# Performance work log

Hardware: AMD Instinct MI355X
Metric: run time of the kernel (lower is better)

The kernel has to match this reference:

```python
import jax, jax.numpy as jnp
import numpy as np

B = 16          # number of point clouds in the batch
N_COARSE = 1024 # coarse points per cloud
N_FINE = 4096   # fine (skip) points per cloud
C_IN = 256
C_SKIP = 128
K = 3
EPS = 1e-16


def setup_inputs() -> dict:
    key = jax.random.key(0)
    ks = jax.random.split(key, 8)
    x = jax.random.normal(ks[0], (B * N_COARSE, C_IN), dtype=jnp.float32)
    pos = jax.random.uniform(ks[1], (B * N_COARSE, 3), dtype=jnp.float32)
    x_skip = jax.random.normal(ks[2], (B * N_FINE, C_SKIP), dtype=jnp.float32)
    pos_skip = jax.random.uniform(ks[3], (B * N_FINE, 3), dtype=jnp.float32)
    batch = jnp.repeat(jnp.arange(B, dtype=jnp.int64), N_COARSE)
    batch_skip = jnp.repeat(jnp.arange(B, dtype=jnp.int64), N_FINE)
    W1 = jax.random.normal(ks[4], (C_IN + C_SKIP, 256), dtype=jnp.float32) * (1.0 / np.sqrt(C_IN + C_SKIP))
    b1 = jnp.zeros((256,), dtype=jnp.float32)
    W2 = jax.random.normal(ks[5], (256, 256), dtype=jnp.float32) * (1.0 / np.sqrt(256))
    b2 = jnp.zeros((256,), dtype=jnp.float32)
    return {"x": x, "pos": pos, "batch": batch, "x_skip": x_skip,
            "pos_skip": pos_skip, "batch_skip": batch_skip,
            "W1": W1, "b1": b1, "W2": W2, "b2": b2}


def _knn_interpolate(x, pos, pos_skip):
    # Equal-sized clouds: reshape to [B, N, *] and do batched kNN.
    xc = x.reshape(B, N_COARSE, C_IN)
    pc = pos.reshape(B, N_COARSE, 3)
    pf = pos_skip.reshape(B, N_FINE, 3)
    # squared pairwise distances [B, M, N]
    d2 = (jnp.sum(pf * pf, -1)[:, :, None]
          + jnp.sum(pc * pc, -1)[:, None, :]
          - 2.0 * jnp.einsum('bmd,bnd->bmn', pf, pc))
    d2 = jnp.maximum(d2, 0.0)
    neg_d2k, idx = jax.lax.top_k(-d2, K)          # k smallest distances
    w = 1.0 / jnp.maximum(-neg_d2k, EPS)          # [B, M, K] inverse-sq-dist weights
    gathered = jax.vmap(lambda f, i: f[i])(xc, idx)  # [B, M, K, C]
    y = jnp.sum(w[..., None] * gathered, axis=2) / jnp.sum(w, axis=2, keepdims=True)
    return y.reshape(B * N_FINE, C_IN)


def reference(x, pos, batch, x_skip, pos_skip, batch_skip, W1, b1, W2, b2):
    x_interp = _knn_interpolate(x, pos, pos_skip)          # [B*M, C_IN]
    h = jnp.concatenate([x_interp, x_skip], axis=1)        # [B*M, C_IN + C_SKIP]
    h = jax.nn.relu(h @ W1 + b1)
    out = jax.nn.relu(h @ W2 + b2)
    return out
```

## Files before the change

kernel.cpp:

```cpp
#include <hip/hip_runtime.h>

typedef float  f32x4  __attribute__((ext_vector_type(4)));
typedef short  short8 __attribute__((ext_vector_type(8)));
typedef unsigned short ushort_t;
typedef ushort_t us4   __attribute__((ext_vector_type(4)));

#define NCOARSE 1024
#define NFINE   4096

#define GLL16(g, l)                                                   \
  __builtin_amdgcn_global_load_lds(                                   \
      (__attribute__((address_space(1))) void*)(g),                   \
      (__attribute__((address_space(3))) void*)(l), 16, 0, 0)

__device__ __forceinline__ ushort_t f2bf(float f){
  union { float f; unsigned u; } a; a.f = f;
  unsigned u = a.u;
  return (ushort_t)((u + 0x7fffu + ((u >> 16) & 1u)) >> 16);
}

__device__ __forceinline__ f32x4 splat4(float v){ f32x4 t = {v, v, v, v}; return t; }

__global__ void prep_w2(const float* __restrict__ W1, const float* __restrict__ W2,
                        ushort_t* __restrict__ W1p, ushort_t* __restrict__ W2p){
  int e = blockIdx.x * 256 + threadIdx.x;
  const float* W; ushort_t* Wp; int idx;
  if (e < 98304){ W = W1; Wp = W1p; idx = e; }
  else          { W = W2; Wp = W2p; idx = e - 98304; }
  int j    = idx & 7;
  int lane = (idx >> 3) & 63;
  int g    = idx >> 9;
  int nb   = g & 15;
  int kc   = g >> 4;
  int k = kc * 32 + (lane >> 4) * 8 + j;
  int n = nb * 16 + (lane & 15);
  Wp[idx] = f2bf(W[k * 256 + n]);
}

__global__ __launch_bounds__(256) void knn_kernel(const float* __restrict__ pos,
                           const float* __restrict__ pos_skip,
                           int* __restrict__ knn_i, float* __restrict__ knn_w){
  __shared__ f32x4 cand[8][129];
  const int tid = threadIdx.x;
  const int b   = blockIdx.x >> 7;
  const int m   = blockIdx.x * 32 + (tid >> 3);
  const int chunk = tid & 7;

  const float* p = pos + (size_t)b * NCOARSE * 3;
  for (int c = tid; c < NCOARSE; c += 256){
    float x = p[3*c], y = p[3*c+1], z = p[3*c+2];
    float sc = __fadd_rn(__fadd_rn(__fmul_rn(x,x), __fmul_rn(y,y)), __fmul_rn(z,z));
    f32x4 v = { x, y, z, sc };
    cand[c >> 7][c & 127] = v;
  }
  __syncthreads();

  const float* q = pos_skip + (size_t)m * 3;
  float qx = q[0], qy = q[1], qz = q[2];
  float sf = __fadd_rn(__fadd_rn(__fmul_rn(qx,qx), __fmul_rn(qy,qy)), __fmul_rn(qz,qz));

  float d0 = 1e30f, d1 = 1e30f, d2 = 1e30f;
  int   i0 = 0,     i1 = 0,     i2 = 0;
  const int gbase = chunk * 128;
  #pragma unroll 4
  for (int i = 0; i < 128; ++i){
    f32x4 v = cand[chunk][i];
    float dot = __fadd_rn(__fadd_rn(__fmul_rn(qx, v.x), __fmul_rn(qy, v.y)),
                          __fmul_rn(qz, v.z));
    float d = __fsub_rn(__fadd_rn(sf, v.w), __fmul_rn(2.0f, dot));
    d = fmaxf(d, 0.0f);
    if (d < d2){
      int gi = gbase + i;
      if (d < d1){
        d2 = d1; i2 = i1;
        if (d < d0){ d1 = d0; i1 = i0; d0 = d; i0 = gi; }
        else       { d1 = d;  i1 = gi; }
      } else { d2 = d; i2 = gi; }
    }
  }

  #pragma unroll
  for (int mlev = 1; mlev <= 4; mlev <<= 1){
    float e0 = __shfl_xor(d0, mlev), e1 = __shfl_xor(d1, mlev), e2 = __shfl_xor(d2, mlev);
    int   j0 = __shfl_xor(i0, mlev), j1 = __shfl_xor(i1, mlev), j2 = __shfl_xor(i2, mlev);
    #pragma unroll
    for (int s = 0; s < 3; ++s){
      float e = (s == 0) ? e0 : (s == 1) ? e1 : e2;
      int   j = (s == 0) ? j0 : (s == 1) ? j1 : j2;
      bool l2 = (e < d2) || (e == d2 && j < i2);
      if (l2){
        bool l1 = (e < d1) || (e == d1 && j < i1);
        if (l1){
          d2 = d1; i2 = i1;
          bool l0 = (e < d0) || (e == d0 && j < i0);
          if (l0){ d1 = d0; i1 = i0; d0 = e; i0 = j; }
          else   { d1 = e;  i1 = j; }
        } else { d2 = e; i2 = j; }
      }
    }
  }

  if (chunk == 0){
    float w0 = 1.0f / fmaxf(d0, 1e-16f);
    float w1 = 1.0f / fmaxf(d1, 1e-16f);
    float w2 = 1.0f / fmaxf(d2, 1e-16f);
    float ws = __fadd_rn(__fadd_rn(w0, w1), w2);
    knn_i[3*m]   = b * NCOARSE + i0;
    knn_i[3*m+1] = b * NCOARSE + i1;
    knn_i[3*m+2] = b * NCOARSE + i2;
    knn_w[3*m]   = w0 / ws;
    knn_w[3*m+1] = w1 / ws;
    knn_w[3*m+2] = w2 / ws;
  }
}

__global__ __launch_bounds__(256, 2)
void fused_fp(const float* __restrict__ x, const float* __restrict__ x_skip,
              const int* __restrict__ knn_i, const float* __restrict__ knn_w,
              const ushort_t* __restrict__ W1p, const float* __restrict__ b1,
              const ushort_t* __restrict__ W2p, const float* __restrict__ b2,
              float* __restrict__ out){
  __shared__ __align__(16) ushort_t hbuf[32 * 384];
  __shared__ __align__(16) ushort_t wbuf[3][8192];
  char* h1b = (char*)hbuf;
  char* h2b = (char*)hbuf;
  const int tid  = threadIdx.x;
  const int lb   = ((blockIdx.x & 7) << 8) + (blockIdx.x >> 3);
  const int row0 = lb * 32;
  const int wp   = tid >> 6;
  const int lane = tid & 63;
  const int lhi  = lane >> 4;
  const int llo  = lane & 15;

  auto stageW = [&](int s){
    const ushort_t* Wsel = (s < 12) ? W1p : W2p;
    int fbase = ((s < 12) ? s : (s - 12)) * 16 + wp * 4;
    #pragma unroll
    for (int i = 0; i < 4; ++i){
      const ushort_t* g = Wsel + (size_t)(fbase + i) * 512 + lane * 8;
      ushort_t* l = &wbuf[s % 3][(wp * 4 + i) * 512];
      GLL16(g, l);
    }
  };

  stageW(0);
  stageW(1);

  {
    const int r   = tid >> 3;
    const int sub = tid & 7;
    const int m   = row0 + r;
    const f32x4* xsr = (const f32x4*)(x_skip + (size_t)m * 128);
    f32x4 xs[4];
    #pragma unroll
    for (int it = 0; it < 4; ++it) xs[it] = xsr[it * 8 + sub];
    int i0 = knn_i[3*m], i1 = knn_i[3*m+1], i2 = knn_i[3*m+2];
    float w0 = knn_w[3*m], w1 = knn_w[3*m+1], w2 = knn_w[3*m+2];
    const f32x4* x0 = (const f32x4*)(x + (size_t)i0 * 256);
    const f32x4* x1 = (const f32x4*)(x + (size_t)i1 * 256);
    const f32x4* x2 = (const f32x4*)(x + (size_t)i2 * 256);
    #pragma unroll
    for (int it = 0; it < 8; ++it){
      int c4 = it * 8 + sub;
      f32x4 v = x0[c4] * w0 + x1[c4] * w1 + x2[c4] * w2;
      int byte = (r * 768 + c4 * 8) ^ ((r & 7) << 4);
      us4 pk = { f2bf(v.x), f2bf(v.y), f2bf(v.z), f2bf(v.w) };
      *(us4*)(h1b + byte) = pk;
    }
    #pragma unroll
    for (int it = 0; it < 4; ++it){
      int c4 = it * 8 + sub;
      f32x4 v = xs[it];
      int byte = (r * 768 + 512 + c4 * 8) ^ ((r & 7) << 4);
      us4 pk = { f2bf(v.x), f2bf(v.y), f2bf(v.z), f2bf(v.w) };
      *(us4*)(h1b + byte) = pk;
    }
  }
  __syncthreads();

  f32x4 acc[2][4];
  #pragma unroll
  for (int nbp = 0; nbp < 4; ++nbp){
    float bb = b1[wp * 64 + nbp * 16 + llo];
    #pragma unroll
    for (int mb = 0; mb < 2; ++mb) acc[mb][nbp] = splat4(bb);
  }
  #pragma unroll
  for (int kk = 0; kk < 12; ++kk){
    asm volatile("s_waitcnt vmcnt(4)" ::: "memory");
    __builtin_amdgcn_s_barrier();
    asm volatile("" ::: "memory");
    stageW(kk + 2);
    short8 af[2];
    #pragma unroll
    for (int mb = 0; mb < 2; ++mb){
      int rr = mb * 16 + llo;
      int byte = (rr * 768 + kk * 64 + lhi * 16) ^ ((rr & 7) << 4);
      af[mb] = *(const short8*)(h1b + byte);
    }
    short8 wf[4];
    #pragma unroll
    for (int nbp = 0; nbp < 4; ++nbp)
      wf[nbp] = *(const short8*)&wbuf[kk % 3][(wp * 4 + nbp) * 512 + lane * 8];
    #pragma unroll
    for (int mb = 0; mb < 2; ++mb)
      #pragma unroll
      for (int nbp = 0; nbp < 4; ++nbp)
        acc[mb][nbp] = __builtin_amdgcn_mfma_f32_16x16x32_bf16(
            af[mb], wf[nbp], acc[mb][nbp], 0, 0, 0);
  }
  __syncthreads();

  #pragma unroll
  for (int mb = 0; mb < 2; ++mb)
    #pragma unroll
    for (int nbp = 0; nbp < 4; ++nbp)
      #pragma unroll
      for (int rg = 0; rg < 4; ++rg){
        int rr  = mb * 16 + lhi * 4 + rg;
        int col = wp * 64 + nbp * 16 + llo;
        int byte = (rr * 512 + col * 2) ^ ((rr & 7) << 4);
        *(ushort_t*)(h2b + byte) = f2bf(fmaxf(acc[mb][nbp][rg], 0.0f));
      }
  __syncthreads();

  f32x4 acc2[2][4];
  #pragma unroll
  for (int nbp = 0; nbp < 4; ++nbp){
    float bb = b2[wp * 64 + nbp * 16 + llo];
    #pragma unroll
    for (int mb = 0; mb < 2; ++mb) acc2[mb][nbp] = splat4(bb);
  }
  #pragma unroll
  for (int t = 0; t < 8; ++t){
    const int s = 12 + t;
    if (t < 7) { asm volatile("s_waitcnt vmcnt(4)" ::: "memory"); }
    else       { asm volatile("s_waitcnt vmcnt(0)" ::: "memory"); }
    __builtin_amdgcn_s_barrier();
    asm volatile("" ::: "memory");
    if (t < 6) stageW(s + 2);
    short8 af[2];
    #pragma unroll
    for (int mb = 0; mb < 2; ++mb){
      int rr = mb * 16 + llo;
      int byte = (rr * 512 + t * 64 + lhi * 16) ^ ((rr & 7) << 4);
      af[mb] = *(const short8*)(h2b + byte);
    }
    short8 wf[4];
    #pragma unroll
    for (int nbp = 0; nbp < 4; ++nbp)
      wf[nbp] = *(const short8*)&wbuf[s % 3][(wp * 4 + nbp) * 512 + lane * 8];
    #pragma unroll
    for (int mb = 0; mb < 2; ++mb)
      #pragma unroll
      for (int nbp = 0; nbp < 4; ++nbp)
        acc2[mb][nbp] = __builtin_amdgcn_mfma_f32_16x16x32_bf16(
            af[mb], wf[nbp], acc2[mb][nbp], 0, 0, 0);
  }

  #pragma unroll
  for (int mb = 0; mb < 2; ++mb)
    #pragma unroll
    for (int nbp = 0; nbp < 4; ++nbp)
      #pragma unroll
      for (int rg = 0; rg < 4; ++rg){
        int row = row0 + mb * 16 + lhi * 4 + rg;
        int col = wp * 64 + nbp * 16 + llo;
        out[(size_t)row * 256 + col] = fmaxf(acc2[mb][nbp][rg], 0.0f);
      }
}

extern "C" void kernel_launch(void* const* d_in, const int* in_sizes, int n_in,
                              void* d_out, int out_size, void* d_ws, size_t ws_size,
                              hipStream_t stream){
  (void)in_sizes; (void)n_in; (void)out_size; (void)ws_size;
  const float* x        = (const float*)d_in[0];
  const float* pos      = (const float*)d_in[1];
  const float* x_skip   = (const float*)d_in[3];
  const float* pos_skip = (const float*)d_in[4];
  const float* W1 = (const float*)d_in[6];
  const float* b1 = (const float*)d_in[7];
  const float* W2 = (const float*)d_in[8];
  const float* b2 = (const float*)d_in[9];
  float* out = (float*)d_out;
  char* ws = (char*)d_ws;
  ushort_t* W1p = (ushort_t*)(ws);
  ushort_t* W2p = (ushort_t*)(ws + 196608);
  int*      ki  = (int*)(ws + 327680);
  float*    kw  = (float*)(ws + 1114112);

  hipLaunchKernelGGL(prep_w2, dim3(640), dim3(256), 0, stream, W1, W2, W1p, W2p);
  hipLaunchKernelGGL(knn_kernel, dim3(2048), dim3(256), 0, stream, pos, pos_skip, ki, kw);
  hipLaunchKernelGGL(fused_fp, dim3(2048), dim3(256), 0, stream,
                     x, x_skip, ki, kw, W1p, b1, W2p, b2, out);
}
```

Before: 96.09 us.

## Fuse kNN search into MLP kernel and load weights directly to registers

Merges the kNN kernel into the fused MLP kernel. Each block now computes its own 32 rows' three nearest neighbours in shared memory, then reuses the same buffer for the activations, so the neighbour index and weight arrays no longer round-trip through global memory and one launch goes away. Weight fragments are also loaded straight from global memory into a three-deep register ring instead of being staged through LDS with barriers, and occupancy is raised to three blocks per CU. The risks are more register pressure and each block repeating the candidate-table load for its cloud.

```diff
diff --git a/kernel.cpp b/kernel.cpp
--- a/kernel.cpp
+++ b/kernel.cpp
@@ -7,11 +7,6 @@
 
 #define NCOARSE 1024
 #define NFINE   4096
-
-#define GLL16(g, l)                                                   \
-  __builtin_amdgcn_global_load_lds(                                   \
-      (__attribute__((address_space(1))) void*)(g),                   \
-      (__attribute__((address_space(3))) void*)(l), 16, 0, 0)
 
 __device__ __forceinline__ ushort_t f2bf(float f){
   union { float f; unsigned u; } a; a.f = f;
@@ -37,132 +32,115 @@
   Wp[idx] = f2bf(W[k * 256 + n]);
 }
 
-__global__ __launch_bounds__(256) void knn_kernel(const float* __restrict__ pos,
-                           const float* __restrict__ pos_skip,
-                           int* __restrict__ knn_i, float* __restrict__ knn_w){
-  __shared__ f32x4 cand[8][129];
-  const int tid = threadIdx.x;
-  const int b   = blockIdx.x >> 7;
-  const int m   = blockIdx.x * 32 + (tid >> 3);
-  const int chunk = tid & 7;
-
-  const float* p = pos + (size_t)b * NCOARSE * 3;
-  for (int c = tid; c < NCOARSE; c += 256){
-    float x = p[3*c], y = p[3*c+1], z = p[3*c+2];
-    float sc = __fadd_rn(__fadd_rn(__fmul_rn(x,x), __fmul_rn(y,y)), __fmul_rn(z,z));
-    f32x4 v = { x, y, z, sc };
-    cand[c >> 7][c & 127] = v;
-  }
-  __syncthreads();
-
-  const float* q = pos_skip + (size_t)m * 3;
-  float qx = q[0], qy = q[1], qz = q[2];
-  float sf = __fadd_rn(__fadd_rn(__fmul_rn(qx,qx), __fmul_rn(qy,qy)), __fmul_rn(qz,qz));
-
-  float d0 = 1e30f, d1 = 1e30f, d2 = 1e30f;
-  int   i0 = 0,     i1 = 0,     i2 = 0;
-  const int gbase = chunk * 128;
-  #pragma unroll 4
-  for (int i = 0; i < 128; ++i){
-    f32x4 v = cand[chunk][i];
-    float dot = __fadd_rn(__fadd_rn(__fmul_rn(qx, v.x), __fmul_rn(qy, v.y)),
-                          __fmul_rn(qz, v.z));
-    float d = __fsub_rn(__fadd_rn(sf, v.w), __fmul_rn(2.0f, dot));
-    d = fmaxf(d, 0.0f);
-    if (d < d2){
-      int gi = gbase + i;
-      if (d < d1){
-        d2 = d1; i2 = i1;
-        if (d < d0){ d1 = d0; i1 = i0; d0 = d; i0 = gi; }
-        else       { d1 = d;  i1 = gi; }
-      } else { d2 = d; i2 = gi; }
-    }
-  }
-
-  #pragma unroll
-  for (int mlev = 1; mlev <= 4; mlev <<= 1){
-    float e0 = __shfl_xor(d0, mlev), e1 = __shfl_xor(d1, mlev), e2 = __shfl_xor(d2, mlev);
-    int   j0 = __shfl_xor(i0, mlev), j1 = __shfl_xor(i1, mlev), j2 = __shfl_xor(i2, mlev);
-    #pragma unroll
-    for (int s = 0; s < 3; ++s){
-      float e = (s == 0) ? e0 : (s == 1) ? e1 : e2;
-      int   j = (s == 0) ? j0 : (s == 1) ? j1 : j2;
-      bool l2 = (e < d2) || (e == d2 && j < i2);
-      if (l2){
-        bool l1 = (e < d1) || (e == d1 && j < i1);
-        if (l1){
+#define LDW4(DST, WP, STEP)                                                   \
+  { _Pragma("unroll")                                                         \
+    for (int n_ = 0; n_ < 4; ++n_)                                            \
+      DST[n_] = *(const short8*)((WP) +                                       \
+          ((size_t)(((STEP) * 16 + wp * 4 + n_) * 64 + lane)) * 8); }
+
+__global__ __launch_bounds__(256, 3)
+void fp_fused(const float* __restrict__ pos, const float* __restrict__ pos_skip,
+              const float* __restrict__ x, const float* __restrict__ x_skip,
+              const ushort_t* __restrict__ W1p, const float* __restrict__ b1,
+              const ushort_t* __restrict__ W2p, const float* __restrict__ b2,
+              float* __restrict__ out){
+  __shared__ __align__(16) ushort_t hbuf[32 * 384];
+  char* h1b = (char*)hbuf;
+  char* h2b = (char*)hbuf;
+  f32x4* candp = (f32x4*)hbuf;
+  const int tid  = threadIdx.x;
+  const int lb   = ((blockIdx.x & 7) << 8) + (blockIdx.x >> 3);
+  const int row0 = lb * 32;
+  const int b    = lb >> 7;
+  const int wp   = tid >> 6;
+  const int lane = tid & 63;
+  const int lhi  = lane >> 4;
+  const int llo  = lane & 15;
+  const int r    = tid >> 3;
+  const int sub  = tid & 7;
+
+  {
+    const float* p = pos + (size_t)b * NCOARSE * 3;
+    for (int c = tid; c < NCOARSE; c += 256){
+      float xx = p[3*c], yy = p[3*c+1], zz = p[3*c+2];
+      float sc = __fadd_rn(__fadd_rn(__fmul_rn(xx,xx), __fmul_rn(yy,yy)), __fmul_rn(zz,zz));
+      f32x4 v = { xx, yy, zz, sc };
+      candp[(c >> 7) * 129 + (c & 127)] = v;
+    }
+  }
+  __syncthreads();
+
+  float wn0, wn1, wn2;
+  int   ig0, ig1, ig2;
+  {
+    const int m = row0 + r;
+    const float* q = pos_skip + (size_t)m * 3;
+    float qx = q[0], qy = q[1], qz = q[2];
+    float sf = __fadd_rn(__fadd_rn(__fmul_rn(qx,qx), __fmul_rn(qy,qy)), __fmul_rn(qz,qz));
+
+    float d0 = 1e30f, d1 = 1e30f, d2 = 1e30f;
+    int   i0 = 0,     i1 = 0,     i2 = 0;
+    const int gbase = sub * 128;
+    #pragma unroll 4
+    for (int i = 0; i < 128; ++i){
+      f32x4 v = candp[sub * 129 + i];
+      float dot = __fadd_rn(__fadd_rn(__fmul_rn(qx, v.x), __fmul_rn(qy, v.y)),
+                            __fmul_rn(qz, v.z));
+      float d = __fsub_rn(__fadd_rn(sf, v.w), __fmul_rn(2.0f, dot));
+      d = fmaxf(d, 0.0f);
+      if (d < d2){
+        int gi = gbase + i;
+        if (d < d1){
           d2 = d1; i2 = i1;
-          bool l0 = (e < d0) || (e == d0 && j < i0);
-          if (l0){ d1 = d0; i1 = i0; d0 = e; i0 = j; }
-          else   { d1 = e;  i1 = j; }
-        } else { d2 = e; i2 = j; }
-      }
-    }
-  }
-
-  if (chunk == 0){
+          if (d < d0){ d1 = d0; i1 = i0; d0 = d; i0 = gi; }
+          else       { d1 = d;  i1 = gi; }
+        } else { d2 = d; i2 = gi; }
+      }
+    }
+
+    #pragma unroll
+    for (int mlev = 1; mlev <= 4; mlev <<= 1){
+      float e0 = __shfl_xor(d0, mlev), e1 = __shfl_xor(d1, mlev), e2 = __shfl_xor(d2, mlev);
+      int   j0 = __shfl_xor(i0, mlev), j1 = __shfl_xor(i1, mlev), j2 = __shfl_xor(i2, mlev);
+      #pragma unroll
+      for (int s = 0; s < 3; ++s){
+        float e = (s == 0) ? e0 : (s == 1) ? e1 : e2;
+        int   j = (s == 0) ? j0 : (s == 1) ? j1 : j2;
+        bool l2 = (e < d2) || (e == d2 && j < i2);
+        if (l2){
+          bool l1 = (e < d1) || (e == d1 && j < i1);
+          if (l1){
+            d2 = d1; i2 = i1;
+            bool l0 = (e < d0) || (e == d0 && j < i0);
+            if (l0){ d1 = d0; i1 = i0; d0 = e; i0 = j; }
+            else   { d1 = e;  i1 = j; }
+          } else { d2 = e; i2 = j; }
+        }
+      }
+    }
+
     float w0 = 1.0f / fmaxf(d0, 1e-16f);
     float w1 = 1.0f / fmaxf(d1, 1e-16f);
     float w2 = 1.0f / fmaxf(d2, 1e-16f);
     float ws = __fadd_rn(__fadd_rn(w0, w1), w2);
-    knn_i[3*m]   = b * NCOARSE + i0;
-    knn_i[3*m+1] = b * NCOARSE + i1;
-    knn_i[3*m+2] = b * NCOARSE + i2;
-    knn_w[3*m]   = w0 / ws;
-    knn_w[3*m+1] = w1 / ws;
-    knn_w[3*m+2] = w2 / ws;
-  }
-}
-
-__global__ __launch_bounds__(256, 2)
-void fused_fp(const float* __restrict__ x, const float* __restrict__ x_skip,
-              const int* __restrict__ knn_i, const float* __restrict__ knn_w,
-              const ushort_t* __restrict__ W1p, const float* __restrict__ b1,
-              const ushort_t* __restrict__ W2p, const float* __restrict__ b2,
-              float* __restrict__ out){
-  __shared__ __align__(16) ushort_t hbuf[32 * 384];
-  __shared__ __align__(16) ushort_t wbuf[3][8192];
-  char* h1b = (char*)hbuf;
-  char* h2b = (char*)hbuf;
-  const int tid  = threadIdx.x;
-  const int lb   = ((blockIdx.x & 7) << 8) + (blockIdx.x >> 3);
-  const int row0 = lb * 32;
-  const int wp   = tid >> 6;
-  const int lane = tid & 63;
-  const int lhi  = lane >> 4;
-  const int llo  = lane & 15;
-
-  auto stageW = [&](int s){
-    const ushort_t* Wsel = (s < 12) ? W1p : W2p;
-    int fbase = ((s < 12) ? s : (s - 12)) * 16 + wp * 4;
-    #pragma unroll
-    for (int i = 0; i < 4; ++i){
-      const ushort_t* g = Wsel + (size_t)(fbase + i) * 512 + lane * 8;
-      ushort_t* l = &wbuf[s % 3][(wp * 4 + i) * 512];
-      GLL16(g, l);
-    }
-  };
-
-  stageW(0);
-  stageW(1);
-
-  {
-    const int r   = tid >> 3;
-    const int sub = tid & 7;
-    const int m   = row0 + r;
+    wn0 = w0 / ws; wn1 = w1 / ws; wn2 = w2 / ws;
+    ig0 = b * NCOARSE + i0; ig1 = b * NCOARSE + i1; ig2 = b * NCOARSE + i2;
+  }
+  __syncthreads();
+
+  {
+    const int m = row0 + r;
     const f32x4* xsr = (const f32x4*)(x_skip + (size_t)m * 128);
     f32x4 xs[4];
     #pragma unroll
     for (int it = 0; it < 4; ++it) xs[it] = xsr[it * 8 + sub];
-    int i0 = knn_i[3*m], i1 = knn_i[3*m+1], i2 = knn_i[3*m+2];
-    float w0 = knn_w[3*m], w1 = knn_w[3*m+1], w2 = knn_w[3*m+2];
-    const f32x4* x0 = (const f32x4*)(x + (size_t)i0 * 256);
-    const f32x4* x1 = (const f32x4*)(x + (size_t)i1 * 256);
-    const f32x4* x2 = (const f32x4*)(x + (size_t)i2 * 256);
+    const f32x4* x0 = (const f32x4*)(x + (size_t)ig0 * 256);
+    const f32x4* x1 = (const f32x4*)(x + (size_t)ig1 * 256);
+    const f32x4* x2 = (const f32x4*)(x + (size_t)ig2 * 256);
     #pragma unroll
     for (int it = 0; it < 8; ++it){
       int c4 = it * 8 + sub;
-      f32x4 v = x0[c4] * w0 + x1[c4] * w1 + x2[c4] * w2;
+      f32x4 v = x0[c4] * wn0 + x1[c4] * wn1 + x2[c4] * wn2;
       int byte = (r * 768 + c4 * 8) ^ ((r & 7) << 4);
       us4 pk = { f2bf(v.x), f2bf(v.y), f2bf(v.z), f2bf(v.w) };
       *(us4*)(h1b + byte) = pk;
@@ -185,29 +163,28 @@
     #pragma unroll
     for (int mb = 0; mb < 2; ++mb) acc[mb][nbp] = splat4(bb);
   }
-  #pragma unroll
-  for (int kk = 0; kk < 12; ++kk){
-    asm volatile("s_waitcnt vmcnt(4)" ::: "memory");
-    __builtin_amdgcn_s_barrier();
-    asm volatile("" ::: "memory");
-    stageW(kk + 2);
-    short8 af[2];
-    #pragma unroll
-    for (int mb = 0; mb < 2; ++mb){
-      int rr = mb * 16 + llo;
-      int byte = (rr * 768 + kk * 64 + lhi * 16) ^ ((rr & 7) << 4);
-      af[mb] = *(const short8*)(h1b + byte);
-    }
-    short8 wf[4];
-    #pragma unroll
-    for (int nbp = 0; nbp < 4; ++nbp)
-      wf[nbp] = *(const short8*)&wbuf[kk % 3][(wp * 4 + nbp) * 512 + lane * 8];
-    #pragma unroll
-    for (int mb = 0; mb < 2; ++mb)
-      #pragma unroll
-      for (int nbp = 0; nbp < 4; ++nbp)
-        acc[mb][nbp] = __builtin_amdgcn_mfma_f32_16x16x32_bf16(
-            af[mb], wf[nbp], acc[mb][nbp], 0, 0, 0);
+  {
+    short8 wr[3][4];
+    LDW4(wr[0], W1p, 0);
+    LDW4(wr[1], W1p, 1);
+    LDW4(wr[2], W1p, 2);
+    #pragma unroll
+    for (int kk = 0; kk < 12; ++kk){
+      short8 af[2];
+      #pragma unroll
+      for (int mb = 0; mb < 2; ++mb){
+        int rr = mb * 16 + llo;
+        int byte = (rr * 768 + kk * 64 + lhi * 16) ^ ((rr & 7) << 4);
+        af[mb] = *(const short8*)(h1b + byte);
+      }
+      #pragma unroll
+      for (int mb = 0; mb < 2; ++mb)
+        #pragma unroll
+        for (int nbp = 0; nbp < 4; ++nbp)
+          acc[mb][nbp] = __builtin_amdgcn_mfma_f32_16x16x32_bf16(
+              af[mb], wr[kk % 3][nbp], acc[mb][nbp], 0, 0, 0);
+      if (kk + 3 < 12) { LDW4(wr[kk % 3], W1p, kk + 3); }
+    }
   }
   __syncthreads();
 
@@ -231,31 +208,28 @@
     #pragma unroll
     for (int mb = 0; mb < 2; ++mb) acc2[mb][nbp] = splat4(bb);
   }
-  #pragma unroll
-  for (int t = 0; t < 8; ++t){
-    const int s = 12 + t;
-    if (t < 7) { asm volatile("s_waitcnt vmcnt(4)" ::: "memory"); }
-    else       { asm volatile("s_waitcnt vmcnt(0)" ::: "memory"); }
-    __builtin_amdgcn_s_barrier();
-    asm volatile("" ::: "memory");
-    if (t < 6) stageW(s + 2);
-    short8 af[2];
-    #pragma unroll
-    for (int mb = 0; mb < 2; ++mb){
-      int rr = mb * 16 + llo;
-      int byte = (rr * 512 + t * 64 + lhi * 16) ^ ((rr & 7) << 4);
-      af[mb] = *(const short8*)(h2b + byte);
-    }
-    short8 wf[4];
-    #pragma unroll
-    for (int nbp = 0; nbp < 4; ++nbp)
-      wf[nbp] = *(const short8*)&wbuf[s % 3][(wp * 4 + nbp) * 512 + lane * 8];
-    #pragma unroll
-    for (int mb = 0; mb < 2; ++mb)
-      #pragma unroll
-      for (int nbp = 0; nbp < 4; ++nbp)
-        acc2[mb][nbp] = __builtin_amdgcn_mfma_f32_16x16x32_bf16(
-            af[mb], wf[nbp], acc2[mb][nbp], 0, 0, 0);
+  {
+    short8 wr[3][4];
+    LDW4(wr[0], W2p, 0);
+    LDW4(wr[1], W2p, 1);
+    LDW4(wr[2], W2p, 2);
+    #pragma unroll
+    for (int kk = 0; kk < 8; ++kk){
+      short8 af[2];
+      #pragma unroll
+      for (int mb = 0; mb < 2; ++mb){
+        int rr = mb * 16 + llo;
+        int byte = (rr * 512 + kk * 64 + lhi * 16) ^ ((rr & 7) << 4);
+        af[mb] = *(const short8*)(h2b + byte);
+      }
+      #pragma unroll
+      for (int mb = 0; mb < 2; ++mb)
+        #pragma unroll
+        for (int nbp = 0; nbp < 4; ++nbp)
+          acc2[mb][nbp] = __builtin_amdgcn_mfma_f32_16x16x32_bf16(
+              af[mb], wr[kk % 3][nbp], acc2[mb][nbp], 0, 0, 0);
+      if (kk + 3 < 8) { LDW4(wr[kk % 3], W2p, kk + 3); }
+    }
   }
 
   #pragma unroll
@@ -286,11 +260,8 @@
   char* ws = (char*)d_ws;
   ushort_t* W1p = (ushort_t*)(ws);
   ushort_t* W2p = (ushort_t*)(ws + 196608);
-  int*      ki  = (int*)(ws + 327680);
-  float*    kw  = (float*)(ws + 1114112);
 
   hipLaunchKernelGGL(prep_w2, dim3(640), dim3(256), 0, stream, W1, W2, W1p, W2p);
-  hipLaunchKernelGGL(knn_kernel, dim3(2048), dim3(256), 0, stream, pos, pos_skip, ki, kw);
-  hipLaunchKernelGGL(fused_fp, dim3(2048), dim3(256), 0, stream,
-                     x, x_skip, ki, kw, W1p, b1, W2p, b2, out);
-}
+  hipLaunchKernelGGL(fp_fused, dim3(2048), dim3(256), 0, stream,
+                     pos, pos_skip, x, x_skip, W1p, b1, W2p, b2, out);
+}
```

Measured after the change: 78.83 us (median of 3 runs). -18.0%, faster.
